# Performance work log

Hardware: AMD Instinct MI355X
Metric: run time of the kernel (lower is better)

The kernel has to match this reference:

```python
import jax, jax.numpy as jnp
import numpy as np

N_NODES = 50000
N_EDGES = 800000


def setup_inputs() -> dict:
    key = jax.random.key(0)
    ks = jax.random.split(key, 8)
    x = jax.random.normal(ks[0], (N_NODES, 128), dtype=jnp.float32)
    edge_src = jax.random.randint(ks[1], (N_EDGES,), 0, N_NODES, dtype=jnp.int32)
    edge_dst = jax.random.randint(ks[2], (N_EDGES,), 0, N_NODES, dtype=jnp.int32)
    # normalized-adjacency-style positive edge weights
    edge_weight = jax.random.uniform(ks[3], (N_EDGES,), dtype=jnp.float32)
    # Kipf-style uniform(-stdv, stdv) init, stdv = 1/sqrt(fan_out)
    def w(k, fi, fo):
        stdv = 1.0 / np.sqrt(fo)
        return jax.random.uniform(k, (fi, fo), minval=-stdv, maxval=stdv, dtype=jnp.float32)
    W1 = w(ks[4], 128, 128)
    W2 = w(ks[5], 128, 128)
    W3 = w(ks[6], 128, 64)
    b1 = jnp.zeros((128,), jnp.float32)
    b2 = jnp.zeros((128,), jnp.float32)
    b3 = jnp.zeros((64,), jnp.float32)
    return {"x": x, "edge_src": edge_src, "edge_dst": edge_dst,
            "edge_weight": edge_weight, "W1": W1, "b1": b1,
            "W2": W2, "b2": b2, "W3": W3, "b3": b3}


def reference(x, edge_src, edge_dst, edge_weight, W1, b1, W2, b2, W3, b3):
    N = x.shape[0]

    def graph_conv(h, W, b):
        # support = h @ W  (dense GEMM)
        support = h @ W
        # spmm(adj, support): gather source rows, scale by edge weight,
        # scatter-add into destination rows
        msg = edge_weight[:, None] * support[edge_src]          # [E, d_out]
        agg = jax.ops.segment_sum(msg, edge_dst, num_segments=N)
        return agg + b

    h = jax.nn.relu(graph_conv(x, W1, b1))
    h = jax.nn.relu(graph_conv(h, W2, b2))
    h = graph_conv(h, W3, b3)
    return jax.nn.log_softmax(h, axis=1)
```

## Files before the change

kernel.cpp:

```cpp
#include <hip/hip_runtime.h>
#include <cstdint>
#include <cstddef>

typedef __attribute__((ext_vector_type(8))) short short8v;
typedef __attribute__((ext_vector_type(4))) float f32x4;

__device__ inline uint bf16_rne(float f) {
    uint u = __float_as_uint(f);
    return (u + 0x7fffu + ((u >> 16) & 1u)) >> 16;
}
__device__ inline float bf16lo_to_f(uint v) { return __uint_as_float(v << 16); }
__device__ inline float bf16hi_to_f(uint v) { return __uint_as_float(v & 0xffff0000u); }

#define MAXDEG 64
#define RSV 384
#define EPB 2048

__device__ inline void pack_one(const float* __restrict__ W, ushort* __restrict__ Wp,
                                int NC, int i) {
    int j = i & 7, l = (i >> 3) & 63, kb = (i >> 9) & 3, c = i >> 11;
    int row = kb * 32 + ((l >> 4) & 3) * 8 + j;
    int col = c * 16 + (l & 15);
    Wp[i] = (ushort)bf16_rne(W[row * NC + col]);
}

__global__ void init_kernel(int* __restrict__ cnt, int N,
                            const float* __restrict__ W1, ushort* __restrict__ Wp1,
                            const float* __restrict__ W2, ushort* __restrict__ Wp2,
                            const float* __restrict__ W3, ushort* __restrict__ Wp3) {
    int i = blockIdx.x * blockDim.x + threadIdx.x;
    if (i < N) cnt[i] = 0;
    int zblocks = (N + 255) >> 8;
    int p = i - zblocks * 256;
    if (p >= 0) {
        if (p < 16384) pack_one(W1, Wp1, 128, p);
        else if (p < 32768) pack_one(W2, Wp2, 128, p - 16384);
        else if (p < 40960) pack_one(W3, Wp3, 64, p - 32768);
    }
}

template <int NC, bool F32IN>
__device__ __forceinline__ void gemm_body(const void* __restrict__ Xin,
                                          const ushort* __restrict__ Wp,
                                          ushort* __restrict__ Out, int M, int bid,
                                          ushort* WL) {
    const int t = threadIdx.x;
    {
        const uint4* srcp = (const uint4*)Wp;
        uint4* dstp = (uint4*)WL;
#pragma unroll
        for (int i = 0; i < NC / 16; ++i) dstp[t + i * 256] = srcp[t + i * 256];
    }
    __syncthreads();

    const int wave = t >> 6, l = t & 63;
    const int lr = l & 15, lh = l >> 4;
    const int rowbase = bid * 64 + wave * 16;
    const int arow_idx = min(rowbase + lr, M - 1);

    short8v a[4];
    if (F32IN) {
        const float* arow = (const float*)Xin + (size_t)arow_idx * 128 + lh * 8;
#pragma unroll
        for (int kb = 0; kb < 4; ++kb) {
            float4 u = *(const float4*)(arow + kb * 32);
            float4 v = *(const float4*)(arow + kb * 32 + 4);
            short8v av;
            av[0] = (short)bf16_rne(u.x); av[1] = (short)bf16_rne(u.y);
            av[2] = (short)bf16_rne(u.z); av[3] = (short)bf16_rne(u.w);
            av[4] = (short)bf16_rne(v.x); av[5] = (short)bf16_rne(v.y);
            av[6] = (short)bf16_rne(v.z); av[7] = (short)bf16_rne(v.w);
            a[kb] = av;
        }
    } else {
        const ushort* arow = (const ushort*)Xin + (size_t)arow_idx * 128 + lh * 8;
#pragma unroll
        for (int kb = 0; kb < 4; ++kb) a[kb] = *(const short8v*)(arow + kb * 32);
    }

    f32x4 acc[NC / 16];
#pragma unroll
    for (int c = 0; c < NC / 16; ++c) acc[c] = (f32x4){0.f, 0.f, 0.f, 0.f};

#pragma unroll
    for (int c = 0; c < NC / 16; ++c)
#pragma unroll
        for (int kb = 0; kb < 4; ++kb) {
            short8v b = *(const short8v*)(WL + ((c * 4 + kb) * 64 + l) * 8);
            acc[c] = __builtin_amdgcn_mfma_f32_16x16x32_bf16(a[kb], b, acc[c], 0, 0, 0);
        }

#pragma unroll
    for (int c = 0; c < NC / 16; ++c)
#pragma unroll
        for (int i = 0; i < 4; ++i) {
            int row = rowbase + lh * 4 + i;
            if (row < M) Out[(size_t)row * NC + c * 16 + lr] = (ushort)bf16_rne(acc[c][i]);
        }
}

template <int NC, bool F32IN>
__global__ __launch_bounds__(256) void gemm_mfma(const void* __restrict__ Xin,
                                                 const ushort* __restrict__ Wp,
                                                 ushort* __restrict__ Out, int M) {
    __shared__ ushort WL[128 * NC];
    gemm_body<NC, F32IN>(Xin, Wp, Out, M, blockIdx.x, WL);
}

__global__ __launch_bounds__(256) void gemm1_part_kernel(
        const float* __restrict__ X, const ushort* __restrict__ Wp1,
        ushort* __restrict__ Out, int M, int GG, int NFG, int TG, int NFB,
        const int* __restrict__ esrc, const int* __restrict__ edst,
        const float* __restrict__ ew, float invN8,
        int* __restrict__ lens, int2* __restrict__ part, int E) {
    __shared__ ushort WL[128 * 128];
    const int g = blockIdx.x >> 3;
    const int i = blockIdx.x & 7;
    const int S = max(1, TG / NFG);
    const bool is_fill = (g % S == 0) && (g / S < NFG);
    if (!is_fill) {
        const int fills_before = min((g + S - 1) / S, NFG);
        gemm_body<128, true>(X, Wp1, Out, M, (g - fills_before) * 8 + i, WL);
        return;
    }
    const int fb = (g / S) * 8 + i;
    if (fb >= NFB) return;
    __shared__ int lcnt[8];
    if (threadIdx.x < 8) lcnt[threadIdx.x] = 0;
    __syncthreads();

    const int lane = threadIdx.x & 63;
    const unsigned long long ltmask = (1ULL << lane) - 1ULL;
    const int base = fb * EPB;

#pragma unroll
    for (int j = 0; j < 8; ++j) {
        int idx = base + j * 256 + threadIdx.x;
        bool valid = idx < E;
        int dv = 0, b = -1;
        int2 rec;
        if (valid) {
            dv = edst[idx];
            b = min(7, (int)((float)dv * invN8));
            rec.x = (dv << 16) | esrc[idx];
            rec.y = __float_as_int(ew[idx]);
        }
        int myrank = 0, lanecnt = 0;
#pragma unroll
        for (int k = 0; k < 8; ++k) {
            unsigned long long mk = __ballot(b == k);
            if (b == k) myrank = (int)__popcll(mk & ltmask);
            if (lane == k) lanecnt = (int)__popcll(mk);
        }
        int wbase = 0;
        if (lane < 8) wbase = atomicAdd(&lcnt[lane], lanecnt);
        int segbase = __shfl(wbase, (b < 0) ? 0 : b);
        if (valid) {
            int pos = segbase + myrank;
            if (pos < RSV) part[((size_t)b * NFB + fb) * RSV + pos] = rec;
        }
    }
    __syncthreads();
    if (threadIdx.x < 8) lens[fb * 8 + threadIdx.x] = min(lcnt[threadIdx.x], RSV);
}

__global__ __launch_bounds__(256) void scatter_kernel(
        const int* __restrict__ lens, const int2* __restrict__ part,
        int* __restrict__ cnt, uint* __restrict__ slots, int NFB) {
    const int bucket = blockIdx.x & 7;
    const int slice = blockIdx.x >> 3;
    const int nsl = gridDim.x >> 3;
    for (int seg = slice; seg < NFB; seg += nsl) {
        const int len = lens[seg * 8 + bucket];
        const int2* p = part + ((size_t)bucket * NFB + seg) * RSV;
        for (int r = threadIdx.x; r < len; r += 256) {
            int2 rec = p[r];
            uint dv = (uint)rec.x >> 16;
            uint src = (uint)rec.x & 0xffffu;
            int pos = atomicAdd(&cnt[dv], 1);
            if (pos < MAXDEG)
                slots[(size_t)dv * MAXDEG + pos] =
                    (bf16_rne(__int_as_float(rec.y)) << 16) | src;
        }
    }
}

__global__ void spmm128_kernel(const uint* __restrict__ S, const int* __restrict__ cnt,
                               const uint* __restrict__ slots, const float* __restrict__ bias,
                               uint* __restrict__ Out, int N) {
    const int node = blockIdx.x * (blockDim.x >> 6) + (threadIdx.x >> 6);
    const int lane = threadIdx.x & 63;
    if (node >= N) return;
    const int e1 = min(cnt[node], MAXDEG);
    const uint* sl = slots + (size_t)node * MAXDEG;
    float ax = 0.f, ay = 0.f;
    int e = 0;

#define EDGE128(pk)                                                  \
    {                                                                \
        uint _p = (pk);                                              \
        float _w = __uint_as_float(_p & 0xffff0000u);                \
        uint _v = S[(size_t)(_p & 0xffffu) * 64 + lane];             \
        ax = fmaf(_w, bf16lo_to_f(_v), ax);                          \
        ay = fmaf(_w, bf16hi_to_f(_v), ay);                          \
    }

    for (; e + 8 <= e1; e += 8) {
        uint4 c0 = *(const uint4*)(sl + e);
        uint4 c1 = *(const uint4*)(sl + e + 4);
        EDGE128(c0.x); EDGE128(c0.y); EDGE128(c0.z); EDGE128(c0.w);
        EDGE128(c1.x); EDGE128(c1.y); EDGE128(c1.z); EDGE128(c1.w);
    }
    for (; e + 4 <= e1; e += 4) {
        uint4 c0 = *(const uint4*)(sl + e);
        EDGE128(c0.x); EDGE128(c0.y); EDGE128(c0.z); EDGE128(c0.w);
    }
    for (; e < e1; ++e) EDGE128(sl[e]);
#undef EDGE128

    float2 bv = ((const float2*)bias)[lane];
    ax = fmaxf(ax + bv.x, 0.f);
    ay = fmaxf(ay + bv.y, 0.f);
    Out[(size_t)node * 64 + lane] = (bf16_rne(ay) << 16) | bf16_rne(ax);
}

__global__ void spmm64_kernel(const uint* __restrict__ S32, const int* __restrict__ cnt,
                              const uint* __restrict__ slots, const float* __restrict__ bias,
                              float* __restrict__ Out, int N) {
    const int node = blockIdx.x * (blockDim.x >> 5) + (threadIdx.x >> 5);
    const int l = threadIdx.x & 31;
    if (node >= N) return;
    const int e1 = min(cnt[node], MAXDEG);
    const uint* sl = slots + (size_t)node * MAXDEG;
    float a0 = 0.f, a1 = 0.f;
    int e = 0;

#define EDGE64(pk)                                                  \
    {                                                               \
        uint _p = (pk);                                             \
        float _w = __uint_as_float(_p & 0xffff0000u);               \
        uint _v = S32[(size_t)(_p & 0xffffu) * 32 + l];             \
        a0 = fmaf(_w, bf16lo_to_f(_v), a0);                         \
        a1 = fmaf(_w, bf16hi_to_f(_v), a1);                         \
    }

    for (; e + 8 <= e1; e += 8) {
        uint4 c0 = *(const uint4*)(sl + e);
        uint4 c1 = *(const uint4*)(sl + e + 4);
        EDGE64(c0.x); EDGE64(c0.y); EDGE64(c0.z); EDGE64(c0.w);
        EDGE64(c1.x); EDGE64(c1.y); EDGE64(c1.z); EDGE64(c1.w);
    }
    for (; e + 4 <= e1; e += 4) {
        uint4 c0 = *(const uint4*)(sl + e);
        EDGE64(c0.x); EDGE64(c0.y); EDGE64(c0.z); EDGE64(c0.w);
    }
    for (; e < e1; ++e) EDGE64(sl[e]);
#undef EDGE64

    float2 bv = ((const float2*)bias)[l];
    float v0 = a0 + bv.x;
    float v1 = a1 + bv.y;
    float m = fmaxf(v0, v1);
#pragma unroll
    for (int d = 16; d >= 1; d >>= 1) m = fmaxf(m, __shfl_xor(m, d));
    float s = __expf(v0 - m) + __expf(v1 - m);
#pragma unroll
    for (int d = 16; d >= 1; d >>= 1) s += __shfl_xor(s, d);
    float ls = __logf(s);
    float2 o;
    o.x = (v0 - m) - ls;
    o.y = (v1 - m) - ls;
    ((float2*)Out)[(size_t)node * 32 + l] = o;
}


extern "C" void kernel_launch(void* const* d_in, const int* in_sizes, int n_in,
                              void* d_out, int out_size, void* d_ws, size_t ws_size,
                              hipStream_t stream) {
    const float* x  = (const float*)d_in[0];
    const int* esrc = (const int*)d_in[1];
    const int* edst = (const int*)d_in[2];
    const float* ew = (const float*)d_in[3];
    const float* W1 = (const float*)d_in[4];
    const float* b1 = (const float*)d_in[5];
    const float* W2 = (const float*)d_in[6];
    const float* b2 = (const float*)d_in[7];
    const float* W3 = (const float*)d_in[8];
    const float* b3 = (const float*)d_in[9];

    const int N = in_sizes[0] / 128;
    const int E = in_sizes[1];

    char* ws = (char*)d_ws;
    auto alloc = [&](size_t bytes) {
        char* p = ws;
        ws += (bytes + 255) & ~(size_t)255;
        return p;
    };
    const int NFB = (E + EPB - 1) / EPB;
    int* cnt     = (int*)alloc((size_t)N * 4);
    int* lens    = (int*)alloc((size_t)(NFB + 8) * 8 * 4);
    uint* slots  = (uint*)alloc((size_t)N * MAXDEG * 4);
    ushort* Sb   = (ushort*)alloc((size_t)N * 128 * 2);
    ushort* Hb   = (ushort*)alloc((size_t)N * 128 * 2);
    ushort* Wp1  = (ushort*)alloc(128 * 128 * 2);
    ushort* Wp2  = (ushort*)alloc(128 * 128 * 2);
    ushort* Wp3  = (ushort*)alloc(128 * 64 * 2);
    (void)ws_size;
    int2* part = (int2*)Hb;

    const int zblocks = (N + 255) / 256;
    init_kernel<<<zblocks + (40960 + 255) / 256, 256, 0, stream>>>(
        cnt, N, W1, Wp1, W2, Wp2, W3, Wp3);

    const int GB = (N + 63) / 64;
    const int GG = (GB + 7) / 8;
    const int NFG = (NFB + 7) / 8;
    const int TG = GG + NFG;
    const float invN8 = 8.0f / (float)N;
    gemm1_part_kernel<<<TG * 8, 256, 0, stream>>>(
        x, Wp1, Sb, N, GG, NFG, TG, NFB, esrc, edst, ew, invN8, lens, part, E);

    scatter_kernel<<<128 * 8, 256, 0, stream>>>(lens, part, cnt, slots, NFB);

    spmm128_kernel<<<(N + 3) / 4, 256, 0, stream>>>((const uint*)Sb, cnt, slots, b1, (uint*)Hb, N);

    gemm_mfma<128, false><<<GB, 256, 0, stream>>>(Hb, Wp2, Sb, N);
    spmm128_kernel<<<(N + 3) / 4, 256, 0, stream>>>((const uint*)Sb, cnt, slots, b2, (uint*)Hb, N);

    gemm_mfma<64, false><<<GB, 256, 0, stream>>>(Hb, Wp3, Sb, N);
    spmm64_kernel<<<(N + 7) / 8, 256, 0, stream>>>((const uint*)Sb, cnt, slots, b3, (float*)d_out, N);
}
```

Before: 168.2 us.

## Fuse partitioning into init kernel, overlap scatter with GEMM1, bucket-interleave SpMM blocks

Edge partitioning now runs in the init kernel alongside zeroing the counters and packing the weights. The scatter into per-node slots is merged into the first GEMM launch, with GEMM and scatter block groups interleaved so that the irregular scatter overlaps the dense compute. This removes one kernel launch and the serial gap between them. SpMM kernels map blockIdx so consecutive blocks cover the 8 node ranges round-robin, likely to spread work across XCDs/L2 partitions in line with the bucketing. This adds interleaving complexity and relies on the scatter not racing with the GEMM, since they touch disjoint buffers.

New measurement: 157.1 us. 1.07x faster.

```diff
diff --git a/kernel.cpp b/kernel.cpp
--- a/kernel.cpp
+++ b/kernel.cpp
@@ -24,19 +24,67 @@
     Wp[i] = (ushort)bf16_rne(W[row * NC + col]);
 }
 
-__global__ void init_kernel(int* __restrict__ cnt, int N,
-                            const float* __restrict__ W1, ushort* __restrict__ Wp1,
-                            const float* __restrict__ W2, ushort* __restrict__ Wp2,
-                            const float* __restrict__ W3, ushort* __restrict__ Wp3) {
-    int i = blockIdx.x * blockDim.x + threadIdx.x;
-    if (i < N) cnt[i] = 0;
-    int zblocks = (N + 255) >> 8;
-    int p = i - zblocks * 256;
-    if (p >= 0) {
-        if (p < 16384) pack_one(W1, Wp1, 128, p);
-        else if (p < 32768) pack_one(W2, Wp2, 128, p - 16384);
-        else if (p < 40960) pack_one(W3, Wp3, 64, p - 32768);
-    }
+__global__ __launch_bounds__(256) void part_init_kernel(
+        const int* __restrict__ esrc, const int* __restrict__ edst,
+        const float* __restrict__ ew, float invN8,
+        int* __restrict__ lens, int2* __restrict__ part, int E, int NFB,
+        int* __restrict__ cnt, int N,
+        const float* __restrict__ W1, ushort* __restrict__ Wp1,
+        const float* __restrict__ W2, ushort* __restrict__ Wp2,
+        const float* __restrict__ W3, ushort* __restrict__ Wp3) {
+    const int b = blockIdx.x;
+    if (b >= NFB) {
+        const int ZB = (N + 255) >> 8;
+        int r = b - NFB;
+        if (r < ZB) {
+            int i = r * 256 + threadIdx.x;
+            if (i < N) cnt[i] = 0;
+        } else {
+            int p = (r - ZB) * 256 + threadIdx.x;
+            if (p < 16384) pack_one(W1, Wp1, 128, p);
+            else if (p < 32768) pack_one(W2, Wp2, 128, p - 16384);
+            else if (p < 40960) pack_one(W3, Wp3, 64, p - 32768);
+        }
+        return;
+    }
+    const int fb = b;
+    __shared__ int lcnt[8];
+    if (threadIdx.x < 8) lcnt[threadIdx.x] = 0;
+    __syncthreads();
+
+    const int lane = threadIdx.x & 63;
+    const unsigned long long ltmask = (1ULL << lane) - 1ULL;
+    const int base = fb * EPB;
+
+#pragma unroll
+    for (int j = 0; j < 8; ++j) {
+        int idx = base + j * 256 + threadIdx.x;
+        bool valid = idx < E;
+        int dv = 0, bk = -1;
+        int2 rec;
+        if (valid) {
+            dv = edst[idx];
+            bk = min(7, (int)((float)dv * invN8));
+            rec.x = (dv << 16) | esrc[idx];
+            rec.y = __float_as_int(ew[idx]);
+        }
+        int myrank = 0, lanecnt = 0;
+#pragma unroll
+        for (int k = 0; k < 8; ++k) {
+            unsigned long long mk = __ballot(bk == k);
+            if (bk == k) myrank = (int)__popcll(mk & ltmask);
+            if (lane == k) lanecnt = (int)__popcll(mk);
+        }
+        int wbase = 0;
+        if (lane < 8) wbase = atomicAdd(&lcnt[lane], lanecnt);
+        int segbase = __shfl(wbase, (bk < 0) ? 0 : bk);
+        if (valid) {
+            int pos = segbase + myrank;
+            if (pos < RSV) part[((size_t)bk * NFB + fb) * RSV + pos] = rec;
+        }
+    }
+    __syncthreads();
+    if (threadIdx.x < 8) lens[fb * 8 + threadIdx.x] = min(lcnt[threadIdx.x], RSV);
 }
 
 template <int NC, bool F32IN>
@@ -107,70 +155,22 @@
     gemm_body<NC, F32IN>(Xin, Wp, Out, M, blockIdx.x, WL);
 }
 
-__global__ __launch_bounds__(256) void gemm1_part_kernel(
+__global__ __launch_bounds__(256) void gemm1_scatter_kernel(
         const float* __restrict__ X, const ushort* __restrict__ Wp1,
-        ushort* __restrict__ Out, int M, int GG, int NFG, int TG, int NFB,
-        const int* __restrict__ esrc, const int* __restrict__ edst,
-        const float* __restrict__ ew, float invN8,
-        int* __restrict__ lens, int2* __restrict__ part, int E) {
+        ushort* __restrict__ Out, int M, int GG, int NSG,
+        const int* __restrict__ lens, const int2* __restrict__ part,
+        int* __restrict__ cnt, uint* __restrict__ slots, int NFB) {
     __shared__ ushort WL[128 * 128];
     const int g = blockIdx.x >> 3;
     const int i = blockIdx.x & 7;
-    const int S = max(1, TG / NFG);
-    const bool is_fill = (g % S == 0) && (g / S < NFG);
-    if (!is_fill) {
-        const int fills_before = min((g + S - 1) / S, NFG);
-        gemm_body<128, true>(X, Wp1, Out, M, (g - fills_before) * 8 + i, WL);
+    if (((g & 1) == 0) && ((g >> 1) < GG)) {
+        gemm_body<128, true>(X, Wp1, Out, M, (g >> 1) * 8 + i, WL);
         return;
     }
-    const int fb = (g / S) * 8 + i;
-    if (fb >= NFB) return;
-    __shared__ int lcnt[8];
-    if (threadIdx.x < 8) lcnt[threadIdx.x] = 0;
-    __syncthreads();
-
-    const int lane = threadIdx.x & 63;
-    const unsigned long long ltmask = (1ULL << lane) - 1ULL;
-    const int base = fb * EPB;
-
-#pragma unroll
-    for (int j = 0; j < 8; ++j) {
-        int idx = base + j * 256 + threadIdx.x;
-        bool valid = idx < E;
-        int dv = 0, b = -1;
-        int2 rec;
-        if (valid) {
-            dv = edst[idx];
-            b = min(7, (int)((float)dv * invN8));
-            rec.x = (dv << 16) | esrc[idx];
-            rec.y = __float_as_int(ew[idx]);
-        }
-        int myrank = 0, lanecnt = 0;
-#pragma unroll
-        for (int k = 0; k < 8; ++k) {
-            unsigned long long mk = __ballot(b == k);
-            if (b == k) myrank = (int)__popcll(mk & ltmask);
-            if (lane == k) lanecnt = (int)__popcll(mk);
-        }
-        int wbase = 0;
-        if (lane < 8) wbase = atomicAdd(&lcnt[lane], lanecnt);
-        int segbase = __shfl(wbase, (b < 0) ? 0 : b);
-        if (valid) {
-            int pos = segbase + myrank;
-            if (pos < RSV) part[((size_t)b * NFB + fb) * RSV + pos] = rec;
-        }
-    }
-    __syncthreads();
-    if (threadIdx.x < 8) lens[fb * 8 + threadIdx.x] = min(lcnt[threadIdx.x], RSV);
-}
-
-__global__ __launch_bounds__(256) void scatter_kernel(
-        const int* __restrict__ lens, const int2* __restrict__ part,
-        int* __restrict__ cnt, uint* __restrict__ slots, int NFB) {
-    const int bucket = blockIdx.x & 7;
-    const int slice = blockIdx.x >> 3;
-    const int nsl = gridDim.x >> 3;
-    for (int seg = slice; seg < NFB; seg += nsl) {
+    const int gemms_before = min((g + 1) >> 1, GG);
+    const int sg = g - gemms_before;
+    const int bucket = i;
+    for (int seg = sg; seg < NFB; seg += NSG) {
         const int len = lens[seg * 8 + bucket];
         const int2* p = part + ((size_t)bucket * NFB + seg) * RSV;
         for (int r = threadIdx.x; r < len; r += 256) {
@@ -188,9 +188,13 @@
 __global__ void spmm128_kernel(const uint* __restrict__ S, const int* __restrict__ cnt,
                                const uint* __restrict__ slots, const float* __restrict__ bias,
                                uint* __restrict__ Out, int N) {
-    const int node = blockIdx.x * (blockDim.x >> 6) + (threadIdx.x >> 6);
+    const int bucket = blockIdx.x & 7;
+    const int bidx = blockIdx.x >> 3;
+    const int lo = (int)((long)bucket * N / 8);
+    const int hi = (int)((long)(bucket + 1) * N / 8);
+    const int node = lo + bidx * 4 + (threadIdx.x >> 6);
     const int lane = threadIdx.x & 63;
-    if (node >= N) return;
+    if (node >= hi) return;
     const int e1 = min(cnt[node], MAXDEG);
     const uint* sl = slots + (size_t)node * MAXDEG;
     float ax = 0.f, ay = 0.f;
@@ -227,9 +231,13 @@
 __global__ void spmm64_kernel(const uint* __restrict__ S32, const int* __restrict__ cnt,
                               const uint* __restrict__ slots, const float* __restrict__ bias,
                               float* __restrict__ Out, int N) {
-    const int node = blockIdx.x * (blockDim.x >> 5) + (threadIdx.x >> 5);
+    const int bucket = blockIdx.x & 7;
+    const int bidx = blockIdx.x >> 3;
+    const int lo = (int)((long)bucket * N / 8);
+    const int hi = (int)((long)(bucket + 1) * N / 8);
+    const int node = lo + bidx * 8 + (threadIdx.x >> 5);
     const int l = threadIdx.x & 31;
-    if (node >= N) return;
+    if (node >= hi) return;
     const int e1 = min(cnt[node], MAXDEG);
     const uint* sl = slots + (size_t)node * MAXDEG;
     float a0 = 0.f, a1 = 0.f;
@@ -309,25 +317,28 @@
     (void)ws_size;
     int2* part = (int2*)Hb;
 
-    const int zblocks = (N + 255) / 256;
-    init_kernel<<<zblocks + (40960 + 255) / 256, 256, 0, stream>>>(
+    const float invN8 = 8.0f / (float)N;
+    const int ZB = (N + 255) / 256;
+    const int PK = (40960 + 255) / 256;
+
+    part_init_kernel<<<NFB + ZB + PK, 256, 0, stream>>>(
+        esrc, edst, ew, invN8, lens, part, E, NFB,
         cnt, N, W1, Wp1, W2, Wp2, W3, Wp3);
 
     const int GB = (N + 63) / 64;
     const int GG = (GB + 7) / 8;
-    const int NFG = (NFB + 7) / 8;
-    const int TG = GG + NFG;
-    const float invN8 = 8.0f / (float)N;
-    gemm1_part_kernel<<<TG * 8, 256, 0, stream>>>(
-        x, Wp1, Sb, N, GG, NFG, TG, NFB, esrc, edst, ew, invN8, lens, part, E);
-
-    scatter_kernel<<<128 * 8, 256, 0, stream>>>(lens, part, cnt, slots, NFB);
-
-    spmm128_kernel<<<(N + 3) / 4, 256, 0, stream>>>((const uint*)Sb, cnt, slots, b1, (uint*)Hb, N);
+    const int NSG = 128;
+    const int TG = GG + NSG;
+    gemm1_scatter_kernel<<<TG * 8, 256, 0, stream>>>(
+        x, Wp1, Sb, N, GG, NSG, lens, part, cnt, slots, NFB);
+
+    const int bpb128 = (((N + 7) / 8) + 3) / 4;
+    spmm128_kernel<<<bpb128 * 8, 256, 0, stream>>>((const uint*)Sb, cnt, slots, b1, (uint*)Hb, N);
 
     gemm_mfma<128, false><<<GB, 256, 0, stream>>>(Hb, Wp2, Sb, N);
-    spmm128_kernel<<<(N + 3) / 4, 256, 0, stream>>>((const uint*)Sb, cnt, slots, b2, (uint*)Hb, N);
+    spmm128_kernel<<<bpb128 * 8, 256, 0, stream>>>((const uint*)Sb, cnt, slots, b2, (uint*)Hb, N);
 
     gemm_mfma<64, false><<<GB, 256, 0, stream>>>(Hb, Wp3, Sb, N);
-    spmm64_kernel<<<(N + 7) / 8, 256, 0, stream>>>((const uint*)Sb, cnt, slots, b3, (float*)d_out, N);
-}
+    const int bpb64 = (((N + 7) / 8) + 7) / 8;
+    spmm64_kernel<<<bpb64 * 8, 256, 0, stream>>>((const uint*)Sb, cnt, slots, b3, (float*)d_out, N);
+}
```
